# Kernel tuning notes

Measured on AMD Instinct MI355X. Metric: run time of the kernel, lower is better.

The kernel has to match this reference:

```python
import jax, jax.numpy as jnp
import numpy as np

B, S, H, E, V, OOV = 64, 400, 512, 256, 50000, 100

def setup_inputs() -> dict:
    key = jax.random.key(0)
    ks = jax.random.split(key, 32)
    p = lambda i, shape: jax.random.normal(ks[i], shape, jnp.float32) * 0.02
    emb = p(0, (V, E)).at[0].set(0.0)  # padding_idx=0
    return dict(
        summaries_in=jax.random.randint(ks[1], (B,), 1, V),
        h0=jax.random.normal(ks[2], (B, H), jnp.float32),
        c0=jax.random.normal(ks[3], (B, H), jnp.float32),
        encoder_out=jax.random.normal(ks[4], (B, S, 2 * H), jnp.float32),
        encoder_features=jax.random.normal(ks[5], (S * B, 2 * H), jnp.float32),
        encoder_mask=jnp.ones((S, B), jnp.float32),
        context=jax.random.normal(ks[6], (B, 2 * H), jnp.float32),
        coverage=jax.random.uniform(ks[7], (S, B), jnp.float32) * 0.01,
        texts_extended=jax.random.randint(ks[8], (S, B), 0, V + OOV),
        oov_size=OOV,
        emb=emb,
        W_feat=p(10, (2 * H, 2 * H)), b_feat=p(11, (2 * H,)),
        W_cov=p(12, (2 * H,)), b_cov=p(13, (2 * H,)),
        w_att=p(14, (2 * H,)), b_att=p(15, ()),
        W_ih=p(16, (4 * H, E)), W_hh=p(17, (4 * H, H)),
        b_ih=p(18, (4 * H,)), b_hh=p(19, (4 * H,)),
        W_ctx=p(20, (E, 2 * H + E)), b_ctx=p(21, (E,)),
        W_pg=p(22, (4 * H + E,)), b_pg=p(23, ()),
        W_o1=p(24, (H, 3 * H)), b_o1=p(25, (H,)),
        W_o2=p(26, (V, H)), b_o2=p(27, (V,)),
    )


def reference(summaries_in, h0, c0, encoder_out, encoder_features, encoder_mask,
              context, coverage, texts_extended, oov_size, emb,
              W_feat, b_feat, W_cov, b_cov, w_att, b_att,
              W_ih, W_hh, b_ih, b_hh, W_ctx, b_ctx, W_pg, b_pg,
              W_o1, b_o1, W_o2, b_o2):
    # embedding + context projection: [B, 2H+E] -> [B, E]
    x = emb[summaries_in]
    ctx_out = jnp.concatenate([context, x], axis=1) @ W_ctx.T + b_ctx
    # single LSTM step (torch gate order i, f, g, o)
    gates = ctx_out @ W_ih.T + b_ih + h0 @ W_hh.T + b_hh
    i, f, g, o = jnp.split(gates, 4, axis=1)
    c = jax.nn.sigmoid(f) * c0 + jax.nn.sigmoid(i) * jnp.tanh(g)
    h = jax.nn.sigmoid(o) * jnp.tanh(c)
    hidden_out = jnp.concatenate([h, c], axis=1)  # [B, 2H]
    # Bahdanau attention with coverage
    dec_feat = hidden_out @ W_feat.T + b_feat                 # [B, 2H]
    ef = encoder_features.reshape(S, B, 2 * H)                # [S, B, 2H]
    cov_feat = coverage[..., None] * W_cov + b_cov            # Linear(1, 2H)
    e = jnp.tanh(ef + dec_feat[None] + cov_feat) @ w_att + b_att  # [S, B]
    a = jax.nn.softmax(e, axis=0) * encoder_mask
    a = a / jnp.sum(a, axis=0, keepdims=True)                 # renormalize (Normalize(0))
    ctx_new = jnp.einsum('sb,bsd->bd', a, encoder_out)        # [B, 2H]
    coverage_next = coverage + a
    # pointer-generator mix
    gen_in = jnp.concatenate([ctx_new, hidden_out, ctx_out], axis=1)  # [B, 4H+E]
    p_gen = jax.nn.sigmoid(gen_in @ W_pg + b_pg)[:, None]             # [B, 1]
    logits = (jnp.concatenate([h, ctx_new], axis=1) @ W_o1.T + b_o1) @ W_o2.T + b_o2
    vocab_dist = p_gen * jax.nn.softmax(logits, axis=1)       # [B, V]
    attn_w = (1.0 - p_gen) * a.T                              # [B, S]
    vd = jnp.concatenate([vocab_dist, jnp.zeros((B, oov_size), vocab_dist.dtype)], axis=1)
    vd = vd.at[jnp.arange(B)[:, None], texts_extended.T].add(attn_w)  # scatter_add copy dist
    return vd, hidden_out, ctx_new, a, coverage_next
```

## Files before the change

kernel.cpp:

```cpp
#include <hip/hip_runtime.h>
#include <cmath>

#define B 64
#define S 400
#define H 512
#define E 256
#define V 50000
#define OOV 100
#define H2 1024
#define VDN (V + OOV)
#define NBLK_V 782
#define SC 50

typedef __attribute__((ext_vector_type(8))) short short8;
typedef __attribute__((ext_vector_type(4))) float f32x4;

__device__ __forceinline__ float wred_sum(float v) {
#pragma unroll
  for (int o = 32; o > 0; o >>= 1) v += __shfl_down(v, o, 64);
  return v;
}
__device__ __forceinline__ float wred_max(float v) {
#pragma unroll
  for (int o = 32; o > 0; o >>= 1) v = fmaxf(v, __shfl_down(v, o, 64));
  return v;
}
__device__ __forceinline__ short f2bf(float f) {
  return __builtin_bit_cast(short, (__bf16)f);
}
__device__ __forceinline__ float bf2f(unsigned short u) {
  unsigned x = (unsigned)u << 16;
  return __builtin_bit_cast(float, x);
}
__device__ __forceinline__ float ftanh(float x) {
  float e = __expf(2.f * x);
  return 1.f - 2.f * __builtin_amdgcn_rcpf(e + 1.f);
}
__device__ __forceinline__ float fsig(float x) {
  return __builtin_amdgcn_rcpf(1.f + __expf(-x));
}

__global__ __launch_bounds__(256) void k_pre(
    const float* __restrict__ b_ctx, const float* __restrict__ b_ih,
    const float* __restrict__ b_hh, const float* __restrict__ b_feat,
    const float* __restrict__ b_o1, const float* __restrict__ context,
    const float* __restrict__ emb, const int* __restrict__ sumin,
    const float* __restrict__ h0, float* __restrict__ ctxoutT4,
    float* __restrict__ gates, float* __restrict__ dfeat,
    float* __restrict__ innerT4, float* __restrict__ catT4,
    float* __restrict__ h0T4, float* __restrict__ Zb) {
  int idx = blockIdx.x * 256 + threadIdx.x;
  if (idx < 64) Zb[idx] = 0.f;
  if (idx < 16384) {
    int j = ((idx >> 8) << 2) + (idx & 3);
    ctxoutT4[idx] = b_ctx[j];
  } else if (idx < 16384 + 131072) {
    int i = idx - 16384;
    int j = i & 2047;
    gates[i] = b_ih[j] + b_hh[j];
  } else if (idx < 16384 + 131072 + 65536) {
    int i = idx - 16384 - 131072;
    dfeat[i] = b_feat[i & 1023];
  } else if (idx < 245760) {
    int i = idx - 16384 - 131072 - 65536;
    int j = ((i >> 8) << 2) + (i & 3);
    innerT4[i] = b_o1[j];
  } else if (idx < 245760 + 81920) {
    int i = idx - 245760;
    int e = i & 3, b = (i >> 2) & 63, q = i >> 8;
    int k = q * 4 + e;
    catT4[i] = (k < 1024) ? context[b * 1024 + k]
                          : emb[(size_t)sumin[b] * 256 + (k - 1024)];
  } else {
    int i = idx - 245760 - 81920;
    int e = i & 3, b = (i >> 2) & 63, q = i >> 8;
    h0T4[i] = h0[b * 512 + q * 4 + e];
  }
}

template <int R, int KC, int OUTMODE>
__global__ __launch_bounds__(256) void k_gemmsk(
    const float* __restrict__ A1, const float* __restrict__ W1, int ldw1, int s1,
    const float* __restrict__ A2, const float* __restrict__ W2, int ldw2,
    float* __restrict__ out, int ldout) {
  const int lane = threadIdx.x;
  const int w = threadIdx.y;
  const int j0 = blockIdx.x * (4 * R) + w * R;
  const float* A;
  const float* W;
  int ldw, kc0;
  if ((int)blockIdx.y < s1) {
    A = A1; W = W1; ldw = ldw1; kc0 = blockIdx.y * KC;
  } else {
    A = A2; W = W2; ldw = ldw2; kc0 = (blockIdx.y - s1) * KC;
  }
  float acc[R];
#pragma unroll
  for (int r = 0; r < R; ++r) acc[r] = 0.f;
  const float* ap = A + (size_t)kc0 * 256 + lane * 4;
  const float* wr[R];
#pragma unroll
  for (int r = 0; r < R; ++r) wr[r] = W + (size_t)(j0 + r) * ldw + kc0 * 4;
#pragma unroll 8
  for (int k4 = 0; k4 < KC; ++k4) {
    float4 av = *(const float4*)(ap + (size_t)k4 * 256);
#pragma unroll
    for (int r = 0; r < R; ++r) {
      float4 wv = *(const float4*)(wr[r] + k4 * 4);
      acc[r] += av.x * wv.x + av.y * wv.y + av.z * wv.z + av.w * wv.w;
    }
  }
#pragma unroll
  for (int r = 0; r < R; ++r) {
    int j = j0 + r;
    if constexpr (OUTMODE == 0)
      atomicAdd(&out[((size_t)(j >> 2) * 64 + lane) * 4 + (j & 3)], acc[r]);
    else
      atomicAdd(&out[(size_t)lane * ldout + j], acc[r]);
  }
}

__global__ __launch_bounds__(256) void k_lstm(const float* __restrict__ gates,
                                              const float* __restrict__ c0,
                                              float* __restrict__ hidden,
                                              float* __restrict__ hcT4) {
  int idx = blockIdx.x * 256 + threadIdx.x;
  int b = idx >> 9, u = idx & 511;
  float gi = gates[(size_t)b * 2048 + u];
  float gf = gates[(size_t)b * 2048 + 512 + u];
  float gg = gates[(size_t)b * 2048 + 1024 + u];
  float go = gates[(size_t)b * 2048 + 1536 + u];
  float c = fsig(gf) * c0[(size_t)b * 512 + u] + fsig(gi) * ftanh(gg);
  float h = fsig(go) * ftanh(c);
  hidden[(size_t)b * H2 + u] = h;
  hidden[(size_t)b * H2 + 512 + u] = c;
  hcT4[((u >> 2) * 64 + b) * 4 + (u & 3)] = h;
  int k = 512 + u;
  hcT4[((k >> 2) * 64 + b) * 4 + (k & 3)] = c;
}

__global__ __launch_bounds__(256) void k_ectx(
    const float* __restrict__ ef, const float* __restrict__ dfeat,
    const float* __restrict__ cov, const float* __restrict__ Wcov,
    const float* __restrict__ bcov, const float* __restrict__ watt,
    const float* __restrict__ batt, const float* __restrict__ mask,
    const float* __restrict__ enc, float* __restrict__ e_x,
    float* __restrict__ Zb, float* __restrict__ partc) {
  const int t = threadIdx.x;
  const int b = blockIdx.x & 63;
  const int q = blockIdx.x >> 6;
  float4 dv = ((const float4*)(dfeat + (size_t)b * H2))[t];
  float4 bc = ((const float4*)bcov)[t];
  float4 wc = ((const float4*)Wcov)[t];
  float4 wa = ((const float4*)watt)[t];
  const float bx = dv.x + bc.x, by = dv.y + bc.y;
  const float bz = dv.z + bc.z, bw = dv.w + bc.w;
  float4 evs[8], encs[8];
  float cvals[8];
#pragma unroll
  for (int i = 0; i < 8; ++i) {
    const int s = q * 8 + i;
    evs[i] = ((const float4*)(ef + (size_t)(s * B + b) * H2))[t];
    encs[i] = ((const float4*)(enc + ((size_t)b * S + s) * H2))[t];
    cvals[i] = cov[s * B + b];
  }
  __shared__ float ered[8][4];
  __shared__ float xS[8];
#pragma unroll
  for (int i = 0; i < 8; ++i) {
    float sum = ftanh(evs[i].x + bx + cvals[i] * wc.x) * wa.x +
                ftanh(evs[i].y + by + cvals[i] * wc.y) * wa.y +
                ftanh(evs[i].z + bz + cvals[i] * wc.z) * wa.z +
                ftanh(evs[i].w + bw + cvals[i] * wc.w) * wa.w;
    sum = wred_sum(sum);
    if ((t & 63) == 0) ered[i][t >> 6] = sum;
  }
  __syncthreads();
  if (t < 64) {
    float x = 0.f;
    if (t < 8) {
      int sb = (q * 8 + t) * B + b;
      float e = ered[t][0] + ered[t][1] + ered[t][2] + ered[t][3] + batt[0];
      x = mask[sb] * __expf(e);
      e_x[sb] = x;
      xS[t] = x;
    }
#pragma unroll
    for (int o = 4; o > 0; o >>= 1) x += __shfl_down(x, o, 64);
    if (t == 0) atomicAdd(&Zb[b], x);
  }
  __syncthreads();
  float4 acc = make_float4(0.f, 0.f, 0.f, 0.f);
#pragma unroll
  for (int i = 0; i < 8; ++i) {
    float x = xS[i];
    acc.x += x * encs[i].x;
    acc.y += x * encs[i].y;
    acc.z += x * encs[i].z;
    acc.w += x * encs[i].w;
  }
  ((float4*)(partc + (size_t)blockIdx.x * H2))[t] = acc;
}

__global__ __launch_bounds__(256) void k_ctxpg(
    const float* __restrict__ partc, const float* __restrict__ e_x,
    const float* __restrict__ Zb, const float* __restrict__ coverage,
    const float* __restrict__ hidden, const float* __restrict__ ctxoutT4,
    const float* __restrict__ Wpg, const float* __restrict__ bpg,
    float* __restrict__ ctx_new, float* __restrict__ ctxT4,
    float* __restrict__ pgen, float* __restrict__ a_out,
    float* __restrict__ cov_out) {
  const int b = blockIdx.x;
  const int t = threadIdx.x;
  const int lane = t & 63, w = t >> 6;
  const float rZ = 1.f / Zb[b];
  const int d = t * 4;
  float4 s = make_float4(0.f, 0.f, 0.f, 0.f);
#pragma unroll 10
  for (int sc = 0; sc < SC; ++sc) {
    float4 v = *(const float4*)(partc + (size_t)(sc * 64 + b) * H2 + d);
    s.x += v.x; s.y += v.y; s.z += v.z; s.w += v.w;
  }
  s.x *= rZ; s.y *= rZ; s.z *= rZ; s.w *= rZ;
  *(float4*)(ctx_new + (size_t)b * H2 + d) = s;
  *(float4*)(ctxT4 + (size_t)t * 256 + b * 4) = s;
#pragma unroll
  for (int i = 0; i < 2; ++i) {
    int sidx = t + i * 256;
    if (sidx < S) {
      int sb = sidx * B + b;
      float av = e_x[sb] * rZ;
      a_out[sb] = av;
      cov_out[sb] = coverage[sb] + av;
    }
  }
  float p = s.x * Wpg[d] + s.y * Wpg[d + 1] + s.z * Wpg[d + 2] + s.w * Wpg[d + 3];
#pragma unroll
  for (int j = 0; j < 4; ++j) {
    int k = t + j * 256;
    p += hidden[(size_t)b * H2 + k] * Wpg[1024 + k];
  }
  p += ctxoutT4[(size_t)(t >> 2) * 256 + b * 4 + (t & 3)] * Wpg[2048 + t];
  p = wred_sum(p);
  __shared__ float red[4];
  if (lane == 0) red[w] = p;
  __syncthreads();
  if (t == 0) {
    float dd = red[0] + red[1] + red[2] + red[3] + bpg[0];
    pgen[b] = fsig(dd);
  }
}

__global__ __launch_bounds__(256) void k_packinner(const float* __restrict__ innerT4,
                                                   short8* __restrict__ packB) {
  int f = blockIdx.x * 256 + threadIdx.x;
  int l = f & 63, bt = (f >> 6) & 3, ks = f >> 8;
  int b = bt * 16 + (l & 15);
  int kbase = ks * 32 + (l >> 4) * 8;
  float4 q0 = *(const float4*)&innerT4[(size_t)(kbase / 4) * 256 + b * 4];
  float4 q1 = *(const float4*)&innerT4[(size_t)(kbase / 4 + 1) * 256 + b * 4];
  short8 frag;
  frag[0] = f2bf(q0.x); frag[1] = f2bf(q0.y);
  frag[2] = f2bf(q0.z); frag[3] = f2bf(q0.w);
  frag[4] = f2bf(q1.x); frag[5] = f2bf(q1.y);
  frag[6] = f2bf(q1.z); frag[7] = f2bf(q1.w);
  packB[f] = frag;
}

__global__ __launch_bounds__(256) void k_mfma_logits(
    const float* __restrict__ W2, const short8* __restrict__ packB,
    const float* __restrict__ bias, unsigned short* __restrict__ logits_bf,
    float* __restrict__ mp, float* __restrict__ zp) {
  const int l = threadIdx.x;
  const int w = threadIdx.y;
  const int jblk = blockIdx.x * 64;
  const int jv = min(jblk + w * 16 + (l & 15), V - 1);
  const float4* wp4 = (const float4*)(W2 + (size_t)jv * 512 + (l >> 4) * 8);

  f32x4 acc0 = {0.f, 0.f, 0.f, 0.f}, acc1 = acc0, acc2 = acc0, acc3 = acc0;
  float4 cw0 = wp4[0], cw1 = wp4[1];
#pragma unroll
  for (int ks = 0; ks < 16; ++ks) {
    float4 nw0, nw1;
    if (ks < 15) { nw0 = wp4[(ks + 1) * 8]; nw1 = wp4[(ks + 1) * 8 + 1]; }
    short8 af;
    af[0] = f2bf(cw0.x); af[1] = f2bf(cw0.y); af[2] = f2bf(cw0.z); af[3] = f2bf(cw0.w);
    af[4] = f2bf(cw1.x); af[5] = f2bf(cw1.y); af[6] = f2bf(cw1.z); af[7] = f2bf(cw1.w);
    short8 b0 = packB[(ks * 4 + 0) * 64 + l];
    short8 b1 = packB[(ks * 4 + 1) * 64 + l];
    short8 b2 = packB[(ks * 4 + 2) * 64 + l];
    short8 b3 = packB[(ks * 4 + 3) * 64 + l];
    acc0 = __builtin_amdgcn_mfma_f32_16x16x32_bf16(af, b0, acc0, 0, 0, 0);
    acc1 = __builtin_amdgcn_mfma_f32_16x16x32_bf16(af, b1, acc1, 0, 0, 0);
    acc2 = __builtin_amdgcn_mfma_f32_16x16x32_bf16(af, b2, acc2, 0, 0, 0);
    acc3 = __builtin_amdgcn_mfma_f32_16x16x32_bf16(af, b3, acc3, 0, 0, 0);
    if (ks < 15) { cw0 = nw0; cw1 = nw1; }
  }

  __shared__ float tile[64][65];
  const int rbase = w * 16 + (l >> 4) * 4;
#pragma unroll
  for (int v = 0; v < 4; ++v) {
    int jl = rbase + v;
    int j = jblk + jl;
    float bv = bias[min(j, V - 1)];
    bool valid = (j < V);
    tile[jl][0 * 16 + (l & 15)] = valid ? acc0[v] + bv : -INFINITY;
    tile[jl][1 * 16 + (l & 15)] = valid ? acc1[v] + bv : -INFINITY;
    tile[jl][2 * 16 + (l & 15)] = valid ? acc2[v] + bv : -INFINITY;
    tile[jl][3 * 16 + (l & 15)] = valid ? acc3[v] + bv : -INFINITY;
  }
  __syncthreads();
  const int t = w * 64 + l;
#pragma unroll
  for (int i = 0; i < 16; ++i) {
    int idx = i * 256 + t;
    int jl = idx & 63;
    int b = idx >> 6;
    int j = jblk + jl;
    if (j < V)
      logits_bf[(size_t)b * V + j] = (unsigned short)f2bf(tile[jl][b]);
  }
  if (t < 64) {
    float m = -INFINITY;
#pragma unroll
    for (int jl = 0; jl < 64; ++jl) m = fmaxf(m, tile[jl][t]);
    float z = 0.f;
#pragma unroll
    for (int jl = 0; jl < 64; ++jl) z += __expf(tile[jl][t] - m);
    mp[(size_t)blockIdx.x * 64 + t] = m;
    zp[(size_t)blockIdx.x * 64 + t] = z;
  }
}

__global__ __launch_bounds__(256) void k_vdms(
    const unsigned short* __restrict__ logits_bf, const float* __restrict__ mp,
    const float* __restrict__ zp, const float* __restrict__ pgen,
    const float* __restrict__ a_out, const int* __restrict__ tex,
    float* __restrict__ out) {
  const int b = blockIdx.x >> 3;
  const int c = blockIdx.x & 7;
  const int t = threadIdx.x;
  const int lane = t & 63, w = t >> 6;
  __shared__ float red[4];
  __shared__ float hist[6272];
  float m = -INFINITY;
  for (int i = t; i < NBLK_V; i += 256) m = fmaxf(m, mp[i * 64 + b]);
  m = wred_max(m);
  if (lane == 0) red[w] = m;
  __syncthreads();
  const float M = fmaxf(fmaxf(red[0], red[1]), fmaxf(red[2], red[3]));
  __syncthreads();
  float z = 0.f;
  for (int i = t; i < NBLK_V; i += 256) z += zp[i * 64 + b] * __expf(mp[i * 64 + b] - M);
  z = wred_sum(z);
  if (lane == 0) red[w] = z;
  __syncthreads();
  const float Z = red[0] + red[1] + red[2] + red[3];
  const float pg = pgen[b];
  const float scale = pg / Z;
  const float wq = 1.f - pg;
  const int v0 = c * 6272;
  const int v1 = min(v0 + 6272, VDN);
  for (int i = t; i < 6272; i += 256) hist[i] = 0.f;
  __syncthreads();
  for (int s = t; s < S; s += 256) {
    int v = tex[s * B + b];
    if (v >= v0 && v < v1) atomicAdd(&hist[v - v0], wq * a_out[s * B + b]);
  }
  __syncthreads();
  for (int v = v0 + t; v < v1; v += 256) {
    float val =
        (v < V) ? scale * __expf(bf2f(logits_bf[(size_t)b * V + v]) - M) : 0.f;
    out[(size_t)b * VDN + v] = val + hist[v - v0];
  }
}

extern "C" void kernel_launch(void* const* d_in, const int* in_sizes, int n_in,
                              void* d_out, int out_size, void* d_ws, size_t ws_size,
                              hipStream_t stream) {
  const int* sumin = (const int*)d_in[0];
  const float* h0 = (const float*)d_in[1];
  const float* c0 = (const float*)d_in[2];
  const float* enc_out = (const float*)d_in[3];
  const float* ef = (const float*)d_in[4];
  const float* mask = (const float*)d_in[5];
  const float* context = (const float*)d_in[6];
  const float* coverage = (const float*)d_in[7];
  const int* tex = (const int*)d_in[8];
  const float* emb = (const float*)d_in[10];
  const float* W_feat = (const float*)d_in[11];
  const float* b_feat = (const float*)d_in[12];
  const float* W_cov = (const float*)d_in[13];
  const float* b_cov = (const float*)d_in[14];
  const float* w_att = (const float*)d_in[15];
  const float* b_att = (const float*)d_in[16];
  const float* W_ih = (const float*)d_in[17];
  const float* W_hh = (const float*)d_in[18];
  const float* b_ih = (const float*)d_in[19];
  const float* b_hh = (const float*)d_in[20];
  const float* W_ctx = (const float*)d_in[21];
  const float* b_ctx = (const float*)d_in[22];
  const float* W_pg = (const float*)d_in[23];
  const float* b_pg = (const float*)d_in[24];
  const float* W_o1 = (const float*)d_in[25];
  const float* b_o1 = (const float*)d_in[26];
  const float* W_o2 = (const float*)d_in[27];
  const float* b_o2 = (const float*)d_in[28];

  float* out = (float*)d_out;
  float* vd = out;
  float* hidden = vd + (size_t)B * VDN;
  float* ctx_new = hidden + (size_t)B * H2;
  float* a_out = ctx_new + (size_t)B * H2;
  float* cov_out = a_out + (size_t)S * B;

  float* ws = (float*)d_ws;
  float* catT4 = ws;
  float* h0T4 = catT4 + 81920;
  float* ctxoutT4 = h0T4 + 32768;
  float* gates = ctxoutT4 + 16384;
  float* hidcatT4 = gates + 131072;
  float* dfeat = hidcatT4 + 65536;
  float* e_x = dfeat + 65536;
  float* ctxnewT4 = e_x + 25600;
  float* innerT4 = ctxnewT4 + 65536;
  float* pgen = innerT4 + 32768;
  float* Zb = pgen + 64;
  float* mp = Zb + 64;
  float* zp = mp + 50048;
  float* packBf = zp + 50048;
  float* logits = packBf + 16384;
  float* partc = logits + 1600064;
  short8* packB = (short8*)packBf;
  unsigned short* logits_bf = (unsigned short*)logits;

  dim3 gblk(64, 4);

  k_pre<<<1408, 256, 0, stream>>>(b_ctx, b_ih, b_hh, b_feat, b_o1, context, emb,
                                  sumin, h0, ctxoutT4, gates, dfeat, innerT4,
                                  catT4, h0T4, Zb);
  k_gemmsk<2, 64, 0><<<dim3(32, 5), gblk, 0, stream>>>(
      catT4, W_ctx, 1280, 5, nullptr, nullptr, 0, ctxoutT4, 0);
  k_gemmsk<2, 64, 1><<<dim3(256, 3), gblk, 0, stream>>>(
      ctxoutT4, W_ih, 256, 1, h0T4, W_hh, 512, gates, 2048);
  k_lstm<<<128, 256, 0, stream>>>(gates, c0, hidden, hidcatT4);
  k_gemmsk<2, 64, 1><<<dim3(128, 4), gblk, 0, stream>>>(
      hidcatT4, W_feat, 1024, 4, nullptr, nullptr, 0, dfeat, 1024);
  k_ectx<<<SC * B, 256, 0, stream>>>(ef, dfeat, coverage, W_cov, b_cov, w_att,
                                     b_att, mask, enc_out, e_x, Zb, partc);
  k_ctxpg<<<B, 256, 0, stream>>>(partc, e_x, Zb, coverage, hidden, ctxoutT4,
                                 W_pg, b_pg, ctx_new, ctxnewT4, pgen, a_out,
                                 cov_out);
  k_gemmsk<2, 64, 0><<<dim3(64, 6), gblk, 0, stream>>>(
      hidcatT4, W_o1, 1536, 2, ctxnewT4, W_o1 + 512, 1536, innerT4, 0);
  k_packinner<<<16, 256, 0, stream>>>(innerT4, packB);
  k_mfma_logits<<<NBLK_V, gblk, 0, stream>>>(W_o2, packB, b_o2, logits_bf, mp, zp);
  k_vdms<<<B * 8, 256, 0, stream>>>(logits_bf, mp, zp, pgen, a_out, tex, vd);
}
```

Baseline: 207.1 us.

## Restructure attention-context kernel to process 40 positions per block with wave-level reductions

The fused attention/context kernel now has each block cover 40 source positions, with each wave handling 10 of them, two at a time. Scores are reduced inside each wave with xor shuffles, so the per-position shared-memory and barrier steps go away. The four waves' context partials are combined in shared memory before writing. This cuts the partial-context buffer from 50 to 10 slices per batch, so the follow-up reduction kernel reads less data. The cost is fewer blocks (640 instead of 3200) and more sequential work per wave, which may lower parallelism and latency hiding on this memory-bound pass.

```diff
diff --git a/kernel.cpp b/kernel.cpp
--- a/kernel.cpp
+++ b/kernel.cpp
@@ -10,7 +10,7 @@
 #define H2 1024
 #define VDN (V + OOV)
 #define NBLK_V 782
-#define SC 50
+#define SC 10
 
 typedef __attribute__((ext_vector_type(8))) short short8;
 typedef __attribute__((ext_vector_type(4))) float f32x4;
@@ -18,11 +18,6 @@
 __device__ __forceinline__ float wred_sum(float v) {
 #pragma unroll
   for (int o = 32; o > 0; o >>= 1) v += __shfl_down(v, o, 64);
-  return v;
-}
-__device__ __forceinline__ float wred_max(float v) {
-#pragma unroll
-  for (int o = 32; o > 0; o >>= 1) v = fmaxf(v, __shfl_down(v, o, 64));
   return v;
 }
 __device__ __forceinline__ short f2bf(float f) {
@@ -38,6 +33,11 @@
 }
 __device__ __forceinline__ float fsig(float x) {
   return __builtin_amdgcn_rcpf(1.f + __expf(-x));
+}
+__device__ __forceinline__ float wred_max(float v) {
+#pragma unroll
+  for (int o = 32; o > 0; o >>= 1) v = fmaxf(v, __shfl_down(v, o, 64));
+  return v;
 }
 
 __global__ __launch_bounds__(256) void k_pre(
@@ -147,59 +147,99 @@
     const float* __restrict__ enc, float* __restrict__ e_x,
     float* __restrict__ Zb, float* __restrict__ partc) {
   const int t = threadIdx.x;
+  const int lane = t & 63;
+  const int w = t >> 6;
   const int b = blockIdx.x & 63;
-  const int q = blockIdx.x >> 6;
-  float4 dv = ((const float4*)(dfeat + (size_t)b * H2))[t];
-  float4 bc = ((const float4*)bcov)[t];
-  float4 wc = ((const float4*)Wcov)[t];
-  float4 wa = ((const float4*)watt)[t];
-  const float bx = dv.x + bc.x, by = dv.y + bc.y;
-  const float bz = dv.z + bc.z, bw = dv.w + bc.w;
-  float4 evs[8], encs[8];
-  float cvals[8];
-#pragma unroll
-  for (int i = 0; i < 8; ++i) {
-    const int s = q * 8 + i;
-    evs[i] = ((const float4*)(ef + (size_t)(s * B + b) * H2))[t];
-    encs[i] = ((const float4*)(enc + ((size_t)b * S + s) * H2))[t];
-    cvals[i] = cov[s * B + b];
-  }
-  __shared__ float ered[8][4];
-  __shared__ float xS[8];
-#pragma unroll
-  for (int i = 0; i < 8; ++i) {
-    float sum = ftanh(evs[i].x + bx + cvals[i] * wc.x) * wa.x +
-                ftanh(evs[i].y + by + cvals[i] * wc.y) * wa.y +
-                ftanh(evs[i].z + bz + cvals[i] * wc.z) * wa.z +
-                ftanh(evs[i].w + bw + cvals[i] * wc.w) * wa.w;
-    sum = wred_sum(sum);
-    if ((t & 63) == 0) ered[i][t >> 6] = sum;
-  }
-  __syncthreads();
-  if (t < 64) {
-    float x = 0.f;
-    if (t < 8) {
-      int sb = (q * 8 + t) * B + b;
-      float e = ered[t][0] + ered[t][1] + ered[t][2] + ered[t][3] + batt[0];
-      x = mask[sb] * __expf(e);
-      e_x[sb] = x;
-      xS[t] = x;
-    }
-#pragma unroll
-    for (int o = 4; o > 0; o >>= 1) x += __shfl_down(x, o, 64);
-    if (t == 0) atomicAdd(&Zb[b], x);
-  }
-  __syncthreads();
-  float4 acc = make_float4(0.f, 0.f, 0.f, 0.f);
-#pragma unroll
-  for (int i = 0; i < 8; ++i) {
-    float x = xS[i];
-    acc.x += x * encs[i].x;
-    acc.y += x * encs[i].y;
-    acc.z += x * encs[i].z;
-    acc.w += x * encs[i].w;
-  }
-  ((float4*)(partc + (size_t)blockIdx.x * H2))[t] = acc;
+  const int g = blockIdx.x >> 6;
+  const int s0 = g * 40 + w * 10;
+  float4 dbc[4], wc4[4], wa4[4];
+  {
+    const float4* dfr = (const float4*)(dfeat + (size_t)b * H2);
+    const float4* bcr = (const float4*)bcov;
+    const float4* wcr = (const float4*)Wcov;
+    const float4* war = (const float4*)watt;
+#pragma unroll
+    for (int k = 0; k < 4; ++k) {
+      int i4 = k * 64 + lane;
+      float4 dv = dfr[i4], bc = bcr[i4];
+      dbc[k] = make_float4(dv.x + bc.x, dv.y + bc.y, dv.z + bc.z, dv.w + bc.w);
+      wc4[k] = wcr[i4];
+      wa4[k] = war[i4];
+    }
+  }
+  const float ba = batt[0];
+  float4 acc[4];
+#pragma unroll
+  for (int k = 0; k < 4; ++k) acc[k] = make_float4(0.f, 0.f, 0.f, 0.f);
+  float zsum = 0.f;
+
+  for (int i = 0; i < 10; i += 2) {
+    const int s1 = s0 + i, s2 = s0 + i + 1;
+    const float4* efr1 = (const float4*)(ef + (size_t)(s1 * B + b) * H2);
+    const float4* efr2 = (const float4*)(ef + (size_t)(s2 * B + b) * H2);
+    const float4* enr1 = (const float4*)(enc + ((size_t)b * S + s1) * H2);
+    const float4* enr2 = (const float4*)(enc + ((size_t)b * S + s2) * H2);
+    float4 a1[4], a2[4], e1[4], e2[4];
+#pragma unroll
+    for (int k = 0; k < 4; ++k) {
+      int i4 = k * 64 + lane;
+      a1[k] = efr1[i4];
+      a2[k] = efr2[i4];
+      e1[k] = enr1[i4];
+      e2[k] = enr2[i4];
+    }
+    const float c1 = cov[s1 * B + b], c2 = cov[s2 * B + b];
+    float d1 = 0.f, d2 = 0.f;
+#pragma unroll
+    for (int k = 0; k < 4; ++k) {
+      d1 += ftanh(a1[k].x + dbc[k].x + c1 * wc4[k].x) * wa4[k].x;
+      d1 += ftanh(a1[k].y + dbc[k].y + c1 * wc4[k].y) * wa4[k].y;
+      d1 += ftanh(a1[k].z + dbc[k].z + c1 * wc4[k].z) * wa4[k].z;
+      d1 += ftanh(a1[k].w + dbc[k].w + c1 * wc4[k].w) * wa4[k].w;
+      d2 += ftanh(a2[k].x + dbc[k].x + c2 * wc4[k].x) * wa4[k].x;
+      d2 += ftanh(a2[k].y + dbc[k].y + c2 * wc4[k].y) * wa4[k].y;
+      d2 += ftanh(a2[k].z + dbc[k].z + c2 * wc4[k].z) * wa4[k].z;
+      d2 += ftanh(a2[k].w + dbc[k].w + c2 * wc4[k].w) * wa4[k].w;
+    }
+#pragma unroll
+    for (int o = 32; o > 0; o >>= 1) {
+      d1 += __shfl_xor(d1, o, 64);
+      d2 += __shfl_xor(d2, o, 64);
+    }
+    const float x1 = mask[s1 * B + b] * __expf(d1 + ba);
+    const float x2 = mask[s2 * B + b] * __expf(d2 + ba);
+    if (lane == 0) {
+      e_x[s1 * B + b] = x1;
+      e_x[s2 * B + b] = x2;
+    }
+    zsum += x1 + x2;
+#pragma unroll
+    for (int k = 0; k < 4; ++k) {
+      acc[k].x += x1 * e1[k].x + x2 * e2[k].x;
+      acc[k].y += x1 * e1[k].y + x2 * e2[k].y;
+      acc[k].z += x1 * e1[k].z + x2 * e2[k].z;
+      acc[k].w += x1 * e1[k].w + x2 * e2[k].w;
+    }
+  }
+  if (lane == 0) atomicAdd(&Zb[b], zsum);
+  __shared__ float4 lacc[4][256];
+#pragma unroll
+  for (int k = 0; k < 4; ++k) lacc[w][lane * 4 + k] = acc[k];
+  __syncthreads();
+  if (w == 0) {
+#pragma unroll
+    for (int k = 0; k < 4; ++k) {
+      float4 s = lacc[0][lane * 4 + k];
+      float4 s1 = lacc[1][lane * 4 + k];
+      float4 s2 = lacc[2][lane * 4 + k];
+      float4 s3 = lacc[3][lane * 4 + k];
+      s.x += s1.x + s2.x + s3.x;
+      s.y += s1.y + s2.y + s3.y;
+      s.z += s1.z + s2.z + s3.z;
+      s.w += s1.w + s2.w + s3.w;
+      ((float4*)(partc + (size_t)blockIdx.x * H2))[k * 64 + lane] = s;
+    }
+  }
 }
 
 __global__ __launch_bounds__(256) void k_ctxpg(
@@ -216,7 +256,7 @@
   const float rZ = 1.f / Zb[b];
   const int d = t * 4;
   float4 s = make_float4(0.f, 0.f, 0.f, 0.f);
-#pragma unroll 10
+#pragma unroll
   for (int sc = 0; sc < SC; ++sc) {
     float4 v = *(const float4*)(partc + (size_t)(sc * 64 + b) * H2 + d);
     s.x += v.x; s.y += v.y; s.z += v.z; s.w += v.w;
```

New measurement: 204.9 us. Within noise of the previous version (-1.1%).
